# Optimization experiments

Measured on AMD Instinct MI355X. Metric: run time of the kernel, lower is better.

The kernel has to match this reference:

```python
import jax, jax.numpy as jnp
import numpy as np

N = 50000       # num_nodes
R = 8           # num_relations
H = 64          # hidden_channels
C = 16          # num_classes
E = 1_600_000   # num edges (avg degree 32)
T = 8192        # number of 'author' target nodes (first T nodes after to_homogeneous)


def setup_inputs() -> dict:
    key = jax.random.key(0)
    ks = jax.random.split(key, 12)
    s = 0.02
    return {
        "edge_index": jax.random.randint(ks[0], (2, E), 0, N),
        "edge_type": jax.random.randint(ks[1], (E,), 0, R),
        "num_target": T,
        # conv1 (featureless: weight is an embedding table [R, N, H], root is [N, H])
        "weight1": jax.random.normal(ks[2], (R, N, H), jnp.float32) * s,
        "root1": jax.random.normal(ks[3], (N, H), jnp.float32) * s,
        "bias1": jnp.zeros((H,), jnp.float32),
        # conv2
        "weight2": jax.random.normal(ks[4], (R, H, H), jnp.float32) * s,
        "root2": jax.random.normal(ks[5], (H, H), jnp.float32) * s,
        "bias2": jnp.zeros((H,), jnp.float32),
        # linear head
        "lin_w": jax.random.normal(ks[6], (H, C), jnp.float32) * s,
        "lin_b": jnp.zeros((C,), jnp.float32),
    }


def reference(edge_index, edge_type, num_target, weight1, root1, bias1,
              weight2, root2, bias2, lin_w, lin_b):
    src, dst = edge_index[0], edge_index[1]
    E_ = src.shape[0]

    # PyG RGCNConv aggregates with MEAN per relation, then sums over relations.
    # Count edges per (dst node, relation) to form the per-relation mean denominator.
    seg = dst * R + edge_type                          # [E] combined (node, relation) id
    cnt = jax.ops.segment_sum(jnp.ones((E_,), jnp.float32), seg, num_segments=N * R)
    scale = (1.0 / jnp.maximum(cnt, 1.0))[seg]         # [E]

    # ---- conv1: x is None -> message = weight1[edge_type][src] (embedding lookup) ----
    m1 = weight1[edge_type, src] * scale[:, None]      # [E, H]
    h1 = jax.ops.segment_sum(m1, dst, num_segments=N)  # [N, H]
    h1 = h1 + root1 + bias1                            # root1[arange(N)] == root1
    h1 = jax.nn.elu(h1)

    # ---- conv2: message = h1[src] @ weight2[edge_type] ----
    # Precompute per-relation node transforms [R, N, H], then gather per edge.
    hr = jnp.einsum('nh,rhk->rnk', h1, weight2)        # [R, N, H]
    m2 = hr[edge_type, src] * scale[:, None]           # [E, H]
    h2 = jax.ops.segment_sum(m2, dst, num_segments=N)  # [N, H]
    h2 = h2 + h1 @ root2 + bias2
    h2 = jax.nn.elu(h2)

    # ---- linear head on the target ('author') node slice ----
    out = h2[:num_target] @ lin_w + lin_b              # [T, C]
    return out
```

## Files before the change

### kernel.cpp

```cpp
#include <hip/hip_runtime.h>

#define NNODES 50000
#define NREL   8
#define HID    64
#define NCLS   16
#define NEDGE  1600000
#define NTGT   8192
#define NBINS  (NNODES * NREL)
#define CHUNK  1024
#define NCHUNK ((NBINS + CHUNK - 1) / CHUNK)

__device__ __forceinline__ float elu1(float x) { return x > 0.f ? x : expm1f(x); }

__device__ __forceinline__ int pack_rec(int src, int rel, int cnt) {
  return src | (rel << 16) | (cnt << 19);
}

__global__ void count_kernel(const int* __restrict__ ei, const int* __restrict__ et,
                             int* __restrict__ cnt, int* __restrict__ epos) {
  int e4 = (blockIdx.x * blockDim.x + threadIdx.x) * 4;
  if (e4 >= NEDGE) return;
  int4 d = *(const int4*)(ei + NEDGE + e4);
  int4 r = *(const int4*)(et + e4);
  int4 p;
  p.x = atomicAdd(&cnt[(d.x * NREL + r.x) << 4], 1);
  p.y = atomicAdd(&cnt[(d.y * NREL + r.y) << 4], 1);
  p.z = atomicAdd(&cnt[(d.z * NREL + r.z) << 4], 1);
  p.w = atomicAdd(&cnt[(d.w * NREL + r.w) << 4], 1);
  *(int4*)(epos + e4) = p;
}

__global__ void chunk_sum_kernel(const int* __restrict__ cnt, int* __restrict__ csum) {
  __shared__ int sw[4];
  int t = threadIdx.x, lane = t & 63, wid = t >> 6;
  int i = blockIdx.x * CHUNK + t * 4;
  int s = 0;
  if (i < NBINS)
    s = cnt[(size_t)(i + 0) << 4] + cnt[(size_t)(i + 1) << 4] +
        cnt[(size_t)(i + 2) << 4] + cnt[(size_t)(i + 3) << 4];
#pragma unroll
  for (int off = 32; off >= 1; off >>= 1) s += __shfl_xor(s, off);
  if (lane == 0) sw[wid] = s;
  __syncthreads();
  if (t == 0) csum[blockIdx.x] = sw[0] + sw[1] + sw[2] + sw[3];
}

__global__ void scan_csum_kernel(const int* __restrict__ csum, int* __restrict__ cbase) {
  __shared__ int sw[8];
  int t = threadIdx.x, lane = t & 63, wid = t >> 6;
  int v0 = (t < NCHUNK) ? csum[t] : 0;
  int v = v0;
#pragma unroll
  for (int off = 1; off < 64; off <<= 1) {
    int u = __shfl_up(v, off);
    if (lane >= off) v += u;
  }
  if (lane == 63) sw[wid] = v;
  __syncthreads();
  if (t == 0) {
    int run = 0;
#pragma unroll
    for (int j = 0; j < 8; ++j) { int x = sw[j]; sw[j] = run; run += x; }
  }
  __syncthreads();
  if (t < NCHUNK) cbase[t] = sw[wid] + (v - v0);
}

__global__ void scan_write_kernel(const int* __restrict__ cnt, const int* __restrict__ cbase,
                                  int* __restrict__ binptr) {
  __shared__ int sw[4];
  int t = threadIdx.x, lane = t & 63, wid = t >> 6;
  int i = blockIdx.x * CHUNK + t * 4;
  int c0 = 0, c1 = 0, c2 = 0, c3 = 0;
  if (i < NBINS) {
    c0 = cnt[(size_t)(i + 0) << 4];
    c1 = cnt[(size_t)(i + 1) << 4];
    c2 = cnt[(size_t)(i + 2) << 4];
    c3 = cnt[(size_t)(i + 3) << 4];
  }
  int p0 = c0, p1 = p0 + c1, p2 = p1 + c2, s = p2 + c3;
  int v = s;
#pragma unroll
  for (int off = 1; off < 64; off <<= 1) {
    int u = __shfl_up(v, off);
    if (lane >= off) v += u;
  }
  if (lane == 63) sw[wid] = v;
  __syncthreads();
  if (t == 0) {
    int run = 0;
#pragma unroll
    for (int j = 0; j < 4; ++j) { int x = sw[j]; sw[j] = run; run += x; }
  }
  __syncthreads();
  if (i < NBINS) {
    int excl = cbase[blockIdx.x] + sw[wid] + (v - s);
    *(int4*)(binptr + i) = make_int4(excl, excl + p0, excl + p1, excl + p2);
  }
  if (blockIdx.x == 0 && t == 0) binptr[NBINS] = NEDGE;
}

__global__ void scatter_kernel(const int* __restrict__ ei, const int* __restrict__ et,
                               const int* __restrict__ epos, const int* __restrict__ binptr,
                               int* __restrict__ epo) {
  int e4 = (blockIdx.x * blockDim.x + threadIdx.x) * 4;
  if (e4 >= NEDGE) return;
  int4 sv = *(const int4*)(ei + e4);
  int4 dv = *(const int4*)(ei + NEDGE + e4);
  int4 rv = *(const int4*)(et + e4);
  int4 pv = *(const int4*)(epos + e4);
  int srcs[4] = {sv.x, sv.y, sv.z, sv.w};
  int dsts[4] = {dv.x, dv.y, dv.z, dv.w};
  int rels[4] = {rv.x, rv.y, rv.z, rv.w};
  int poss[4] = {pv.x, pv.y, pv.z, pv.w};
#pragma unroll
  for (int j = 0; j < 4; ++j) {
    int bin = dsts[j] * NREL + rels[j];
    int b = binptr[bin];
    int c = binptr[bin + 1] - b;
    epo[b + poss[j]] = pack_rec(srcs[j], rels[j], c);
  }
}

__global__ __launch_bounds__(256) void conv1_kernel(
    const int* __restrict__ binptr, const int* __restrict__ epo,
    const float* __restrict__ w1, const float* __restrict__ root1,
    const float* __restrict__ bias1, float* __restrict__ h1) {
  int wave = blockIdx.x * 4 + (threadIdx.x >> 6);
  if (wave >= NNODES) return;
  int lane = threadIdx.x & 63;
  int g = lane >> 4;
  int col = (lane & 15) << 2;
  int b0 = binptr[wave * NREL], b8 = binptr[wave * NREL + NREL];
  float4 acc = make_float4(0.f, 0.f, 0.f, 0.f);
  for (int eb = b0; eb < b8; eb += 64) {
    int mb = min(64, b8 - eb);
    int q = epo[eb + min(lane, mb - 1)];
    for (int j = 0; j < mb; j += 32) {
      float4 a[8]; float sc[8];
#pragma unroll
      for (int u = 0; u < 8; ++u) {
        int e0 = j + u * 4;
        if (e0 < mb) {
          int ei = e0 + g;
          int eic = min(ei, mb - 1);
          int rec = __shfl(q, eic);
          int src = rec & 0xFFFF;
          int rel = (rec >> 16) & 7;
          int cnt = ((unsigned)rec) >> 19;
          float s = 1.0f / (float)cnt;
          sc[u] = (ei < mb) ? s : 0.f;
          a[u] = *(const float4*)(w1 + (((size_t)(unsigned)(rel * NNODES + src)) << 6) + col);
        } else {
          sc[u] = 0.f;
          a[u] = make_float4(0.f, 0.f, 0.f, 0.f);
        }
      }
#pragma unroll
      for (int u = 0; u < 8; ++u) {
        acc.x = fmaf(a[u].x, sc[u], acc.x);
        acc.y = fmaf(a[u].y, sc[u], acc.y);
        acc.z = fmaf(a[u].z, sc[u], acc.z);
        acc.w = fmaf(a[u].w, sc[u], acc.w);
      }
    }
  }
#pragma unroll
  for (int off = 16; off < 64; off <<= 1) {
    acc.x += __shfl_xor(acc.x, off);
    acc.y += __shfl_xor(acc.y, off);
    acc.z += __shfl_xor(acc.z, off);
    acc.w += __shfl_xor(acc.w, off);
  }
  if (g == 0) {
    const float* rp = root1 + (((size_t)wave) << 6) + col;
    float4 r = *(const float4*)rp;
    float4 bz = *(const float4*)(bias1 + col);
    float4 v;
    v.x = elu1(acc.x + r.x + bz.x);
    v.y = elu1(acc.y + r.y + bz.y);
    v.z = elu1(acc.z + r.z + bz.z);
    v.w = elu1(acc.w + r.w + bz.w);
    *(float4*)(h1 + (((size_t)wave) << 6) + col) = v;
  }
}

__global__ __launch_bounds__(256) void conv2a_kernel(
    const int* __restrict__ binptr, const int* __restrict__ epo,
    const float* __restrict__ h1, float* __restrict__ agg, int nodeBase, int nloc) {
  int wv = blockIdx.x * 4 + (threadIdx.x >> 6);
  if (wv >= nloc * NREL) return;
  int lane = threadIdx.x & 63;
  int g = lane >> 4;
  int col = (lane & 15) << 2;
  int r = wv & 7;
  int bin = (nodeBase + (wv >> 3)) * NREL + r;
  int bb = binptr[bin], ee = binptr[bin + 1];
  float4 s = make_float4(0.f, 0.f, 0.f, 0.f);
  for (int e = bb; e < ee; e += 64) {
    int mb = min(64, ee - e);
    int q = epo[e + min(lane, mb - 1)];
    for (int j = 0; j < mb; j += 16) {
      float4 a[4]; float vld[4];
#pragma unroll
      for (int u = 0; u < 4; ++u) {
        int e0 = j + u * 4;
        if (e0 < mb) {
          int ei = e0 + g;
          int eic = min(ei, mb - 1);
          int src = __shfl(q, eic) & 0xFFFF;
          vld[u] = (ei < mb) ? 1.f : 0.f;
          a[u] = *(const float4*)(h1 + (((size_t)(unsigned)src) << 6) + col);
        } else {
          vld[u] = 0.f;
          a[u] = make_float4(0.f, 0.f, 0.f, 0.f);
        }
      }
#pragma unroll
      for (int u = 0; u < 4; ++u) {
        s.x = fmaf(a[u].x, vld[u], s.x);
        s.y = fmaf(a[u].y, vld[u], s.y);
        s.z = fmaf(a[u].z, vld[u], s.z);
        s.w = fmaf(a[u].w, vld[u], s.w);
      }
    }
  }
#pragma unroll
  for (int off = 16; off < 64; off <<= 1) {
    s.x += __shfl_xor(s.x, off);
    s.y += __shfl_xor(s.y, off);
    s.z += __shfl_xor(s.z, off);
    s.w += __shfl_xor(s.w, off);
  }
  if (g == 0) {
    float scl = (ee > bb) ? 1.0f / (float)(ee - bb) : 0.f;
    float4 o = make_float4(s.x * scl, s.y * scl, s.z * scl, s.w * scl);
    *(float4*)(agg + (((size_t)wv) << 6) + col) = o;
  }
}

__global__ __launch_bounds__(256, 4) void conv2b_kernel(
    const float* __restrict__ agg, const float* __restrict__ h1,
    const float* __restrict__ w2, const float* __restrict__ root2,
    const float* __restrict__ bias2, const float* __restrict__ lin_w,
    const float* __restrict__ lin_b, float* __restrict__ out, int nodeBase) {
  __shared__ float sW[HID * HID];
  int t = threadIdx.x, lane = t & 63, wid = t >> 6;
  int ln0 = blockIdx.x * 8 + wid * 2;
  float bz = bias2[lane];
  float o0 = bz, o1 = bz;
  for (int r = 0; r < NREL; ++r) {
    if (r) __syncthreads();
#pragma unroll
    for (int i = 0; i < 4; ++i)
      *(float4*)(sW + t * 4 + i * 1024) = *(const float4*)(w2 + (r << 12) + t * 4 + i * 1024);
    __syncthreads();
    const float* a0 = agg + (((size_t)((ln0 + 0) * NREL + r)) << 6);
    const float* a1 = agg + (((size_t)((ln0 + 1) * NREL + r)) << 6);
#pragma unroll 16
    for (int k = 0; k < HID; ++k) {
      float w = sW[(k << 6) + lane];
      o0 = fmaf(a0[k], w, o0);
      o1 = fmaf(a1[k], w, o1);
    }
  }
  __syncthreads();
#pragma unroll
  for (int i = 0; i < 4; ++i)
    *(float4*)(sW + t * 4 + i * 1024) = *(const float4*)(root2 + t * 4 + i * 1024);
  __syncthreads();
  int g0 = nodeBase + ln0;
  const float* r0p = h1 + ((size_t)(g0 + 0) << 6);
  const float* r1p = h1 + ((size_t)(g0 + 1) << 6);
#pragma unroll 16
  for (int k = 0; k < HID; ++k) {
    float w = sW[(k << 6) + lane];
    o0 = fmaf(r0p[k], w, o0);
    o1 = fmaf(r1p[k], w, o1);
  }
  __syncthreads();
  int row0 = wid * 2;
  sW[row0 * 65 + lane] = elu1(o0);
  sW[(row0 + 1) * 65 + lane] = elu1(o1);
  float* lw = sW + 8 * 65;
  *(float4*)(lw + t * 4) = *(const float4*)(lin_w + t * 4);
  __syncthreads();
  if (t < 8 * NCLS) {
    int n = t >> 4, c = t & 15;
    float accv = lin_b[c];
#pragma unroll 16
    for (int l = 0; l < HID; ++l)
      accv = fmaf(sW[n * 65 + l], lw[l * NCLS + c], accv);
    out[((size_t)(nodeBase + blockIdx.x * 8 + n)) * NCLS + c] = accv;
  }
}

extern "C" void kernel_launch(void* const* d_in, const int* in_sizes, int n_in,
                              void* d_out, int out_size, void* d_ws, size_t ws_size,
                              hipStream_t stream) {
  const int*   ei    = (const int*)d_in[0];
  const int*   et    = (const int*)d_in[1];
  const float* w1    = (const float*)d_in[3];
  const float* root1 = (const float*)d_in[4];
  const float* bias1 = (const float*)d_in[5];
  const float* w2    = (const float*)d_in[6];
  const float* root2 = (const float*)d_in[7];
  const float* bias2 = (const float*)d_in[8];
  const float* lin_w = (const float*)d_in[9];
  const float* lin_b = (const float*)d_in[10];
  float* out = (float*)d_out;

  char* ws = (char*)d_ws;
  int*   epos   = (int*)ws;
  char*  p      = ws + (size_t)NEDGE * 4;
  int*   binptr = (int*)p;  p += ((size_t)(NBINS + 1) * 4 + 255) & ~(size_t)255;
  int*   csum   = (int*)p;  p += ((size_t)NCHUNK * 4 + 255) & ~(size_t)255;
  int*   cbase  = (int*)p;  p += ((size_t)NCHUNK * 4 + 255) & ~(size_t)255;
  int*   cnt    = (int*)p;
  float* h1     = (float*)p;
  char*  q      = p + (size_t)NNODES * HID * 4;
  int*   epo    = (int*)q;  q += (size_t)NEDGE * 4;
  float* agg    = (float*)q;
  size_t cnt_end = (size_t)((p + (size_t)NBINS * 64) - ws);
  size_t agg_end = (size_t)(q - ws) + (size_t)NTGT * NREL * HID * 4;
  size_t need8k  = (agg_end > cnt_end) ? agg_end : cnt_end;
  int chunk = (need8k <= ws_size) ? NTGT : NTGT / 2;

  hipMemsetAsync(cnt, 0, (size_t)NBINS * 64, stream);
  count_kernel<<<(NEDGE / 4 + 255) / 256, 256, 0, stream>>>(ei, et, cnt, epos);
  chunk_sum_kernel<<<NCHUNK, 256, 0, stream>>>(cnt, csum);
  scan_csum_kernel<<<1, 512, 0, stream>>>(csum, cbase);
  scan_write_kernel<<<NCHUNK, 256, 0, stream>>>(cnt, cbase, binptr);
  scatter_kernel<<<(NEDGE / 4 + 255) / 256, 256, 0, stream>>>(ei, et, epos, binptr, epo);
  conv1_kernel<<<(NNODES + 3) / 4, 256, 0, stream>>>(binptr, epo, w1, root1, bias1, h1);
  for (int c = 0; c < NTGT / chunk; ++c) {
    conv2a_kernel<<<(chunk * NREL) / 4, 256, 0, stream>>>(binptr, epo, h1, agg, c * chunk, chunk);
    conv2b_kernel<<<chunk / 8, 256, 0, stream>>>(agg, h1, w2, root2, bias2, lin_w, lin_b,
                                                 out, c * chunk);
  }
}
```

Measured before the change: 410.3 us.

## Fuse all pipeline stages into one persistent cooperative kernel with grid syncs

Replaces the memset and chain of count, scan, scatter, conv1, conv2a and conv2b launches with a single cooperative mega-kernel that walks each stage with grid-stride loops separated by grid.sync. The aim is to remove per-launch overhead and inter-kernel idle gaps. It trades this for a capped persistent grid (at most 2048 blocks), which may lower memory-level parallelism in the gather-heavy phases, and for grid-barrier costs. The original multi-kernel path remains as a fallback, now with a fixed two-half split for conv2.

```diff
diff --git a/kernel.cpp b/kernel.cpp
--- a/kernel.cpp
+++ b/kernel.cpp
@@ -1,4 +1,7 @@
 #include <hip/hip_runtime.h>
+#include <hip/hip_cooperative_groups.h>
+
+namespace cg = cooperative_groups;
 
 #define NNODES 50000
 #define NREL   8
@@ -6,6 +9,7 @@
 #define NCLS   16
 #define NEDGE  1600000
 #define NTGT   8192
+#define HALF   4096
 #define NBINS  (NNODES * NREL)
 #define CHUNK  1024
 #define NCHUNK ((NBINS + CHUNK - 1) / CHUNK)
@@ -14,6 +18,298 @@
 
 __device__ __forceinline__ int pack_rec(int src, int rel, int cnt) {
   return src | (rel << 16) | (cnt << 19);
+}
+
+__global__ __launch_bounds__(256) void mega_kernel(
+    const int* __restrict__ ei, const int* __restrict__ et,
+    const float* __restrict__ w1, const float* __restrict__ root1,
+    const float* __restrict__ bias1, const float* __restrict__ w2,
+    const float* __restrict__ root2, const float* __restrict__ bias2,
+    const float* __restrict__ lin_w, const float* __restrict__ lin_b,
+    float* __restrict__ out,
+    int* __restrict__ epos, int* __restrict__ binptr,
+    int* __restrict__ csum, int* __restrict__ cbase,
+    int* cnt, float* h1, int* epo, float* agg) {
+  cg::grid_group grid = cg::this_grid();
+  __shared__ float sW[HID * HID];
+  __shared__ int sw[8];
+  const int t = threadIdx.x, lane = t & 63, wid4 = t >> 6;
+  const int bid = blockIdx.x, G = gridDim.x;
+  const int gtid = bid * 256 + t, nthreads = G * 256;
+  const int gwid = bid * 4 + wid4, nwaves = G * 4;
+
+  for (int i = gtid; i < NBINS * 4; i += nthreads)
+    ((int4*)cnt)[i] = make_int4(0, 0, 0, 0);
+  grid.sync();
+
+  for (int i = gtid; i < NEDGE / 4; i += nthreads) {
+    int e4 = i * 4;
+    int4 d = *(const int4*)(ei + NEDGE + e4);
+    int4 r = *(const int4*)(et + e4);
+    int4 p;
+    p.x = atomicAdd(&cnt[(d.x * NREL + r.x) << 4], 1);
+    p.y = atomicAdd(&cnt[(d.y * NREL + r.y) << 4], 1);
+    p.z = atomicAdd(&cnt[(d.z * NREL + r.z) << 4], 1);
+    p.w = atomicAdd(&cnt[(d.w * NREL + r.w) << 4], 1);
+    *(int4*)(epos + e4) = p;
+  }
+  grid.sync();
+
+  for (int c = bid; c < NCHUNK; c += G) {
+    int i = c * CHUNK + t * 4;
+    int s = 0;
+    if (i < NBINS)
+      s = cnt[(size_t)(i + 0) << 4] + cnt[(size_t)(i + 1) << 4] +
+          cnt[(size_t)(i + 2) << 4] + cnt[(size_t)(i + 3) << 4];
+#pragma unroll
+    for (int off = 32; off >= 1; off >>= 1) s += __shfl_xor(s, off);
+    if (lane == 0) sw[wid4] = s;
+    __syncthreads();
+    if (t == 0) csum[c] = sw[0] + sw[1] + sw[2] + sw[3];
+    __syncthreads();
+  }
+  grid.sync();
+
+  if (bid == 0) {
+    int e0 = t * 2, e1 = t * 2 + 1;
+    int s0 = (e0 < NCHUNK) ? csum[e0] : 0;
+    int s1 = (e1 < NCHUNK) ? csum[e1] : 0;
+    int tsum = s0 + s1;
+    int v = tsum;
+#pragma unroll
+    for (int off = 1; off < 64; off <<= 1) {
+      int u = __shfl_up(v, off);
+      if (lane >= off) v += u;
+    }
+    if (lane == 63) sw[wid4] = v;
+    __syncthreads();
+    if (t == 0) {
+      int run = 0;
+#pragma unroll
+      for (int j = 0; j < 4; ++j) { int x = sw[j]; sw[j] = run; run += x; }
+    }
+    __syncthreads();
+    int base = sw[wid4] + (v - tsum);
+    if (e0 < NCHUNK) cbase[e0] = base;
+    if (e1 < NCHUNK) cbase[e1] = base + s0;
+  }
+  grid.sync();
+
+  for (int c = bid; c < NCHUNK; c += G) {
+    int i = c * CHUNK + t * 4;
+    int c0 = 0, c1 = 0, c2 = 0, c3 = 0;
+    if (i < NBINS) {
+      c0 = cnt[(size_t)(i + 0) << 4];
+      c1 = cnt[(size_t)(i + 1) << 4];
+      c2 = cnt[(size_t)(i + 2) << 4];
+      c3 = cnt[(size_t)(i + 3) << 4];
+    }
+    int p0 = c0, p1 = p0 + c1, p2 = p1 + c2, s = p2 + c3;
+    int v = s;
+#pragma unroll
+    for (int off = 1; off < 64; off <<= 1) {
+      int u = __shfl_up(v, off);
+      if (lane >= off) v += u;
+    }
+    if (lane == 63) sw[wid4] = v;
+    __syncthreads();
+    if (t == 0) {
+      int run = 0;
+#pragma unroll
+      for (int j = 0; j < 4; ++j) { int x = sw[j]; sw[j] = run; run += x; }
+    }
+    __syncthreads();
+    if (i < NBINS) {
+      int excl = cbase[c] + sw[wid4] + (v - s);
+      *(int4*)(binptr + i) = make_int4(excl, excl + p0, excl + p1, excl + p2);
+    }
+    __syncthreads();
+  }
+  if (gtid == 0) binptr[NBINS] = NEDGE;
+  grid.sync();
+
+  for (int i = gtid; i < NEDGE / 4; i += nthreads) {
+    int e4 = i * 4;
+    int4 sv = *(const int4*)(ei + e4);
+    int4 dv = *(const int4*)(ei + NEDGE + e4);
+    int4 rv = *(const int4*)(et + e4);
+    int4 pv = *(const int4*)(epos + e4);
+    int srcs[4] = {sv.x, sv.y, sv.z, sv.w};
+    int dsts[4] = {dv.x, dv.y, dv.z, dv.w};
+    int rels[4] = {rv.x, rv.y, rv.z, rv.w};
+    int poss[4] = {pv.x, pv.y, pv.z, pv.w};
+#pragma unroll
+    for (int j = 0; j < 4; ++j) {
+      int bin = dsts[j] * NREL + rels[j];
+      int b = binptr[bin];
+      int c = binptr[bin + 1] - b;
+      epo[b + poss[j]] = pack_rec(srcs[j], rels[j], c);
+    }
+  }
+  grid.sync();
+
+  {
+    int g = lane >> 4, col = (lane & 15) << 2;
+    for (int node = gwid; node < NNODES; node += nwaves) {
+      int b0 = binptr[node * NREL], b8 = binptr[node * NREL + NREL];
+      float4 acc = make_float4(0.f, 0.f, 0.f, 0.f);
+      for (int eb = b0; eb < b8; eb += 64) {
+        int mb = min(64, b8 - eb);
+        int q = epo[eb + min(lane, mb - 1)];
+        for (int j = 0; j < mb; j += 32) {
+          float4 a[8]; float sc[8];
+#pragma unroll
+          for (int u = 0; u < 8; ++u) {
+            int e0 = j + u * 4;
+            if (e0 < mb) {
+              int ei2 = e0 + g;
+              int eic = min(ei2, mb - 1);
+              int rec = __shfl(q, eic);
+              int src = rec & 0xFFFF;
+              int rel = (rec >> 16) & 7;
+              int cntv = ((unsigned)rec) >> 19;
+              float s = 1.0f / (float)cntv;
+              sc[u] = (ei2 < mb) ? s : 0.f;
+              a[u] = *(const float4*)(w1 + (((size_t)(unsigned)(rel * NNODES + src)) << 6) + col);
+            } else {
+              sc[u] = 0.f;
+              a[u] = make_float4(0.f, 0.f, 0.f, 0.f);
+            }
+          }
+#pragma unroll
+          for (int u = 0; u < 8; ++u) {
+            acc.x = fmaf(a[u].x, sc[u], acc.x);
+            acc.y = fmaf(a[u].y, sc[u], acc.y);
+            acc.z = fmaf(a[u].z, sc[u], acc.z);
+            acc.w = fmaf(a[u].w, sc[u], acc.w);
+          }
+        }
+      }
+#pragma unroll
+      for (int off = 16; off < 64; off <<= 1) {
+        acc.x += __shfl_xor(acc.x, off);
+        acc.y += __shfl_xor(acc.y, off);
+        acc.z += __shfl_xor(acc.z, off);
+        acc.w += __shfl_xor(acc.w, off);
+      }
+      if (g == 0) {
+        float4 r = *(const float4*)(root1 + (((size_t)node) << 6) + col);
+        float4 bz = *(const float4*)(bias1 + col);
+        float4 v;
+        v.x = elu1(acc.x + r.x + bz.x);
+        v.y = elu1(acc.y + r.y + bz.y);
+        v.z = elu1(acc.z + r.z + bz.z);
+        v.w = elu1(acc.w + r.w + bz.w);
+        *(float4*)(h1 + (((size_t)node) << 6) + col) = v;
+      }
+    }
+  }
+  grid.sync();
+
+  for (int half = 0; half < 2; ++half) {
+    int nodeBase = half * HALF;
+    {
+      int g = lane >> 4, col = (lane & 15) << 2;
+      for (int wv = gwid; wv < HALF * NREL; wv += nwaves) {
+        int r = wv & 7;
+        int bin = (nodeBase + (wv >> 3)) * NREL + r;
+        int bb = binptr[bin], ee = binptr[bin + 1];
+        float4 s = make_float4(0.f, 0.f, 0.f, 0.f);
+        for (int e = bb; e < ee; e += 64) {
+          int mb = min(64, ee - e);
+          int q = epo[e + min(lane, mb - 1)];
+          for (int j = 0; j < mb; j += 16) {
+            float4 a[4]; float vld[4];
+#pragma unroll
+            for (int u = 0; u < 4; ++u) {
+              int e0 = j + u * 4;
+              if (e0 < mb) {
+                int ei2 = e0 + g;
+                int eic = min(ei2, mb - 1);
+                int src = __shfl(q, eic) & 0xFFFF;
+                vld[u] = (ei2 < mb) ? 1.f : 0.f;
+                a[u] = *(const float4*)(h1 + (((size_t)(unsigned)src) << 6) + col);
+              } else {
+                vld[u] = 0.f;
+                a[u] = make_float4(0.f, 0.f, 0.f, 0.f);
+              }
+            }
+#pragma unroll
+            for (int u = 0; u < 4; ++u) {
+              s.x = fmaf(a[u].x, vld[u], s.x);
+              s.y = fmaf(a[u].y, vld[u], s.y);
+              s.z = fmaf(a[u].z, vld[u], s.z);
+              s.w = fmaf(a[u].w, vld[u], s.w);
+            }
+          }
+        }
+#pragma unroll
+        for (int off = 16; off < 64; off <<= 1) {
+          s.x += __shfl_xor(s.x, off);
+          s.y += __shfl_xor(s.y, off);
+          s.z += __shfl_xor(s.z, off);
+          s.w += __shfl_xor(s.w, off);
+        }
+        if (g == 0) {
+          float scl = (ee > bb) ? 1.0f / (float)(ee - bb) : 0.f;
+          *(float4*)(agg + (((size_t)wv) << 6) + col) =
+              make_float4(s.x * scl, s.y * scl, s.z * scl, s.w * scl);
+        }
+      }
+    }
+    grid.sync();
+    for (int bt = bid; bt < HALF / 8; bt += G) {
+      int ln0 = bt * 8 + wid4 * 2;
+      float bz = bias2[lane];
+      float o0 = bz, o1 = bz;
+      for (int r = 0; r < NREL; ++r) {
+        if (r) __syncthreads();
+#pragma unroll
+        for (int i = 0; i < 4; ++i)
+          *(float4*)(sW + t * 4 + i * 1024) = *(const float4*)(w2 + (r << 12) + t * 4 + i * 1024);
+        __syncthreads();
+        const float* a0 = agg + (((size_t)((ln0 + 0) * NREL + r)) << 6);
+        const float* a1 = agg + (((size_t)((ln0 + 1) * NREL + r)) << 6);
+#pragma unroll 16
+        for (int k = 0; k < HID; ++k) {
+          float w = sW[(k << 6) + lane];
+          o0 = fmaf(a0[k], w, o0);
+          o1 = fmaf(a1[k], w, o1);
+        }
+      }
+      __syncthreads();
+#pragma unroll
+      for (int i = 0; i < 4; ++i)
+        *(float4*)(sW + t * 4 + i * 1024) = *(const float4*)(root2 + t * 4 + i * 1024);
+      __syncthreads();
+      int g0 = nodeBase + ln0;
+      const float* r0p = h1 + ((size_t)(g0 + 0) << 6);
+      const float* r1p = h1 + ((size_t)(g0 + 1) << 6);
+#pragma unroll 16
+      for (int k = 0; k < HID; ++k) {
+        float w = sW[(k << 6) + lane];
+        o0 = fmaf(r0p[k], w, o0);
+        o1 = fmaf(r1p[k], w, o1);
+      }
+      __syncthreads();
+      int row0 = wid4 * 2;
+      sW[row0 * 65 + lane] = elu1(o0);
+      sW[(row0 + 1) * 65 + lane] = elu1(o1);
+      float* lw = sW + 8 * 65;
+      *(float4*)(lw + t * 4) = *(const float4*)(lin_w + t * 4);
+      __syncthreads();
+      if (t < 8 * NCLS) {
+        int n = t >> 4, c = t & 15;
+        float accv = lin_b[c];
+#pragma unroll 16
+        for (int l = 0; l < HID; ++l)
+          accv = fmaf(sW[n * 65 + l], lw[l * NCLS + c], accv);
+        out[((size_t)(nodeBase + bt * 8 + n)) * NCLS + c] = accv;
+      }
+      __syncthreads();
+    }
+    grid.sync();
+  }
 }
 
 __global__ void count_kernel(const int* __restrict__ ei, const int* __restrict__ et,
@@ -173,8 +469,7 @@
     acc.w += __shfl_xor(acc.w, off);
   }
   if (g == 0) {
-    const float* rp = root1 + (((size_t)wave) << 6) + col;
-    float4 r = *(const float4*)rp;
+    float4 r = *(const float4*)(root1 + (((size_t)wave) << 6) + col);
     float4 bz = *(const float4*)(bias1 + col);
     float4 v;
     v.x = elu1(acc.x + r.x + bz.x);
@@ -234,8 +529,8 @@
   }
   if (g == 0) {
     float scl = (ee > bb) ? 1.0f / (float)(ee - bb) : 0.f;
-    float4 o = make_float4(s.x * scl, s.y * scl, s.z * scl, s.w * scl);
-    *(float4*)(agg + (((size_t)wv) << 6) + col) = o;
+    *(float4*)(agg + (((size_t)wv) << 6) + col) =
+        make_float4(s.x * scl, s.y * scl, s.z * scl, s.w * scl);
   }
 }
 
@@ -321,10 +616,26 @@
   char*  q      = p + (size_t)NNODES * HID * 4;
   int*   epo    = (int*)q;  q += (size_t)NEDGE * 4;
   float* agg    = (float*)q;
-  size_t cnt_end = (size_t)((p + (size_t)NBINS * 64) - ws);
-  size_t agg_end = (size_t)(q - ws) + (size_t)NTGT * NREL * HID * 4;
-  size_t need8k  = (agg_end > cnt_end) ? agg_end : cnt_end;
-  int chunk = (need8k <= ws_size) ? NTGT : NTGT / 2;
+
+  hipError_t lerr = hipErrorUnknown;
+  int coop = 0, dev = 0;
+  (void)hipGetDevice(&dev);
+  if (hipDeviceGetAttribute(&coop, hipDeviceAttributeCooperativeLaunch, dev) == hipSuccess &&
+      coop) {
+    int maxB = 0;
+    hipError_t qerr = hipOccupancyMaxActiveBlocksPerMultiprocessor(&maxB, mega_kernel, 256, 0);
+    if (qerr == hipSuccess && maxB >= 1) {
+      int G = maxB * 256;
+      if (G > 2048) G = 2048;
+      void* args[] = {(void*)&ei, (void*)&et, (void*)&w1, (void*)&root1, (void*)&bias1,
+                      (void*)&w2, (void*)&root2, (void*)&bias2, (void*)&lin_w, (void*)&lin_b,
+                      (void*)&out, (void*)&epos, (void*)&binptr, (void*)&csum, (void*)&cbase,
+                      (void*)&cnt, (void*)&h1, (void*)&epo, (void*)&agg};
+      lerr = hipLaunchCooperativeKernel((void*)mega_kernel, dim3(G), dim3(256), args, 0, stream);
+    }
+  }
+  if (lerr == hipSuccess) return;
+  (void)hipGetLastError();
 
   hipMemsetAsync(cnt, 0, (size_t)NBINS * 64, stream);
   count_kernel<<<(NEDGE / 4 + 255) / 256, 256, 0, stream>>>(ei, et, cnt, epos);
@@ -333,9 +644,9 @@
   scan_write_kernel<<<NCHUNK, 256, 0, stream>>>(cnt, cbase, binptr);
   scatter_kernel<<<(NEDGE / 4 + 255) / 256, 256, 0, stream>>>(ei, et, epos, binptr, epo);
   conv1_kernel<<<(NNODES + 3) / 4, 256, 0, stream>>>(binptr, epo, w1, root1, bias1, h1);
-  for (int c = 0; c < NTGT / chunk; ++c) {
-    conv2a_kernel<<<(chunk * NREL) / 4, 256, 0, stream>>>(binptr, epo, h1, agg, c * chunk, chunk);
-    conv2b_kernel<<<chunk / 8, 256, 0, stream>>>(agg, h1, w2, root2, bias2, lin_w, lin_b,
-                                                 out, c * chunk);
-  }
-}
+  for (int c = 0; c < 2; ++c) {
+    conv2a_kernel<<<(HALF * NREL) / 4, 256, 0, stream>>>(binptr, epo, h1, agg, c * HALF, HALF);
+    conv2b_kernel<<<HALF / 8, 256, 0, stream>>>(agg, h1, w2, root2, bias2, lin_w, lin_b,
+                                                out, c * HALF);
+  }
+}
```

New measurement: 1.012 ms. 147% more time.
